# Kernel optimization log

Measured on AMD Instinct MI355X. Metric: run time of the kernel, lower is better.

The kernel has to match this reference:

```python
import jax, jax.numpy as jnp
import numpy as np

N = 100000          # nodes
E = 1600000         # edges (avg degree 16)
D_IN = 128
D_OUT = 128
K = 3               # Chebyshev order
LAMBDA_MAX = 2.0    # PyG default for sym normalization


def setup_inputs() -> dict:
    key = jax.random.key(0)
    k1, k2, k3, k4 = jax.random.split(key, 4)
    x = jax.random.normal(k1, (N, D_IN), dtype=jnp.float32)
    edge_index = jax.random.randint(k2, (2, E), 0, N, dtype=jnp.int32)
    # Glorot-ish init for the K per-order linear weights
    weight = jax.random.normal(k3, (K, D_IN, D_OUT), dtype=jnp.float32) * (1.0 / np.sqrt(D_IN))
    bias = jax.random.normal(k4, (D_OUT,), dtype=jnp.float32) * 0.01
    return {"x": x, "edge_index": edge_index, "weight": weight, "bias": bias}


def reference(x, edge_index, weight, bias):
    src, dst = edge_index[0], edge_index[1]
    n = x.shape[0]

    # remove self loops (zero their weight), symmetric normalization
    ew = jnp.where(src != dst, 1.0, 0.0).astype(x.dtype)
    deg = jax.ops.segment_sum(ew, src, num_segments=n)
    dis = jnp.where(deg > 0, jax.lax.rsqrt(jnp.maximum(deg, 1.0)), 0.0)
    norm = dis[src] * ew * dis[dst]          # D^-1/2 A D^-1/2 entries

    # scaled Laplacian T-hat = (2/lmax) L - I, L = I - A_norm
    off_w = -(2.0 / LAMBDA_MAX) * norm       # off-diagonal entries
    diag_w = 2.0 / LAMBDA_MAX - 1.0          # = 0 for lambda_max=2

    def spmm(h):  # T-hat @ h : gather-multiply-scatter over edges
        agg = jax.ops.segment_sum(off_w[:, None] * h[src], dst, num_segments=n)
        return agg + diag_w * h

    # Chebyshev recurrence: Tx_k = 2 T-hat Tx_{k-1} - Tx_{k-2}
    Tx0 = x
    out = Tx0 @ weight[0]
    Tx1 = spmm(Tx0)
    out = out + Tx1 @ weight[1]
    for k in range(2, weight.shape[0]):
        Tx2 = 2.0 * spmm(Tx1) - Tx0
        out = out + Tx2 @ weight[k]
        Tx0, Tx1 = Tx1, Tx2
    return out + bias
```

## Files before the change

### kernel.cpp

```cpp
#include <hip/hip_runtime.h>
#include <hip/hip_bf16.h>

typedef __hip_bfloat16 bf16;
typedef __attribute__((ext_vector_type(8))) short short8;
typedef __attribute__((ext_vector_type(4))) float float4v;

#define N_NODES 100000
#define M_PAD   100096
#define N_EDGES 1600000
#define D 128
#define K_CAT 384
#define BUCKET_CAP 64
#define NBIN 392
#define BIN_CAP 4608
#define CHUNK 4096

__device__ __forceinline__ float b2f(bf16 v) { return __bfloat162float(v); }
__device__ __forceinline__ bf16 f2b(float v) { return __float2bfloat16(v); }
__device__ __forceinline__ float us2f(unsigned short u) {
    unsigned int x = ((unsigned int)u) << 16;
    return __uint_as_float(x);
}

__global__ void prep_w_kernel(const float* __restrict__ w, const float* __restrict__ bias,
                              bf16* __restrict__ wT, float* __restrict__ biasf) {
    int i = blockIdx.x * blockDim.x + threadIdx.x;
    if (i < D * K_CAT) {
        int o = i / K_CAT, k = i % K_CAT;
        float v;
        if (k < 128) {
            v = w[k * D + o] - w[2 * 16384 + k * D + o];
        } else if (k < 256) {
            v = w[16384 + (k - 128) * D + o];
        } else {
            v = 2.0f * w[2 * 16384 + (k - 256) * D + o];
        }
        wT[i] = f2b(v);
    }
    if (i < D) biasf[i] = bias[i];
}

__global__ __launch_bounds__(256) void convx_kernel(const float* __restrict__ x,
                                                    bf16* __restrict__ xb) {
    int i = (blockIdx.x * 256 + threadIdx.x) * 4;
    float4 v = *(const float4*)(x + i);
    unsigned int p0 = (unsigned int)__bfloat16_as_ushort(f2b(v.x)) |
                      ((unsigned int)__bfloat16_as_ushort(f2b(v.y)) << 16);
    unsigned int p1 = (unsigned int)__bfloat16_as_ushort(f2b(v.z)) |
                      ((unsigned int)__bfloat16_as_ushort(f2b(v.w)) << 16);
    uint2 pk; pk.x = p0; pk.y = p1;
    *(uint2*)(xb + i) = pk;
}

__global__ __launch_bounds__(256) void phaseA_kernel(const int* __restrict__ src,
                                                     const int* __restrict__ dst,
                                                     int* __restrict__ gCursD,
                                                     int* __restrict__ gCursS,
                                                     unsigned int* __restrict__ gBinD,
                                                     unsigned char* __restrict__ gBinS) {
    __shared__ int histD[NBIN], histS[NBIN], cursD[NBIN], cursS[NBIN];
    int tid = threadIdx.x;
    for (int t = tid; t < NBIN; t += 256) { histD[t] = 0; histS[t] = 0; }
    __syncthreads();
    int e0 = blockIdx.x * CHUNK;
    for (int i = tid; i < CHUNK; i += 256) {
        int e = e0 + i;
        if (e >= N_EDGES) break;
        int s = src[e], d = dst[e];
        if (s == d) continue;
        atomicAdd(&histD[d >> 8], 1);
        atomicAdd(&histS[s >> 8], 1);
    }
    __syncthreads();
    for (int t = tid; t < NBIN; t += 256) {
        cursD[t] = (histD[t] > 0) ? atomicAdd(&gCursD[t], histD[t]) : 0;
        cursS[t] = (histS[t] > 0) ? atomicAdd(&gCursS[t], histS[t]) : 0;
    }
    __syncthreads();
    for (int i = tid; i < CHUNK; i += 256) {
        int e = e0 + i;
        if (e >= N_EDGES) break;
        int s = src[e], d = dst[e];
        if (s == d) continue;
        int bd = d >> 8, bs = s >> 8;
        int sd = atomicAdd(&cursD[bd], 1);
        if (sd < BIN_CAP) gBinD[(size_t)bd * BIN_CAP + sd] = ((unsigned int)s << 8) | (unsigned int)(d & 255);
        int ss = atomicAdd(&cursS[bs], 1);
        if (ss < BIN_CAP) gBinS[(size_t)bs * BIN_CAP + ss] = (unsigned char)(s & 255);
    }
}

__global__ __launch_bounds__(256) void phaseB_kernel(const int* __restrict__ gCursD,
                                                     const int* __restrict__ gCursS,
                                                     const unsigned int* __restrict__ gBinD,
                                                     const unsigned char* __restrict__ gBinS,
                                                     int* __restrict__ cnt,
                                                     float* __restrict__ dis,
                                                     int* __restrict__ bucket) {
    __shared__ int curs[256];
    int tid = threadIdx.x;
    int b = blockIdx.x;
    curs[tid] = 0;
    __syncthreads();
    if (b < NBIN) {
        int count = min(gCursD[b], BIN_CAP);
        const unsigned int* rec = gBinD + (size_t)b * BIN_CAP;
        int n0 = b << 8;
        for (int j = tid; j < count; j += 256) {
            unsigned int r = rec[j];
            int dloc = r & 255;
            int s = (int)(r >> 8);
            int slot = atomicAdd(&curs[dloc], 1);
            if (slot < BUCKET_CAP) bucket[(size_t)(n0 + dloc) * BUCKET_CAP + slot] = s;
        }
        __syncthreads();
        int n = n0 + tid;
        if (n < N_NODES) cnt[n] = curs[tid];
    } else {
        int bb = b - NBIN;
        int count = min(gCursS[bb], BIN_CAP);
        const unsigned char* rec = gBinS + (size_t)bb * BIN_CAP;
        for (int j = tid; j < count; j += 256) {
            atomicAdd(&curs[rec[j]], 1);
        }
        __syncthreads();
        int n = (bb << 8) + tid;
        if (n < N_NODES) {
            int c = curs[tid];
            dis[n] = (c > 0) ? rsqrtf((float)c) : 0.0f;
        }
    }
}

__global__ __launch_bounds__(256) void spmm_kernel(const bf16* __restrict__ h,
                                                   const float* __restrict__ dis,
                                                   const int* __restrict__ cnt,
                                                   const int* __restrict__ bucket,
                                                   bf16* __restrict__ outp) {
    int wv = threadIdx.x >> 6;
    int lane = threadIdx.x & 63;
    int n = blockIdx.x * 4 + wv;
    int c = min(cnt[n], BUCKET_CAP);
    float dn = dis[n];
    int s_l = 0;
    float w_l = 0.0f;
    if (lane < c) {
        s_l = bucket[n * BUCKET_CAP + lane];
        w_l = -dis[s_l] * dn;
    }
    int f0 = lane * 2;
    float ax = 0.0f, ay = 0.0f;
    int j = 0;
    for (; j + 4 <= c; j += 4) {
        int s0 = __shfl(s_l, j + 0), s1 = __shfl(s_l, j + 1);
        int s2 = __shfl(s_l, j + 2), s3 = __shfl(s_l, j + 3);
        float w0 = __shfl(w_l, j + 0), w1 = __shfl(w_l, j + 1);
        float w2 = __shfl(w_l, j + 2), w3 = __shfl(w_l, j + 3);
        unsigned int u0 = *(const unsigned int*)(h + (size_t)s0 * D + f0);
        unsigned int u1 = *(const unsigned int*)(h + (size_t)s1 * D + f0);
        unsigned int u2 = *(const unsigned int*)(h + (size_t)s2 * D + f0);
        unsigned int u3 = *(const unsigned int*)(h + (size_t)s3 * D + f0);
        ax += w0 * us2f((unsigned short)(u0 & 0xffff)) + w1 * us2f((unsigned short)(u1 & 0xffff))
            + w2 * us2f((unsigned short)(u2 & 0xffff)) + w3 * us2f((unsigned short)(u3 & 0xffff));
        ay += w0 * us2f((unsigned short)(u0 >> 16)) + w1 * us2f((unsigned short)(u1 >> 16))
            + w2 * us2f((unsigned short)(u2 >> 16)) + w3 * us2f((unsigned short)(u3 >> 16));
    }
    for (; j < c; j++) {
        int sj = __shfl(s_l, j);
        float wj = __shfl(w_l, j);
        unsigned int u = *(const unsigned int*)(h + (size_t)sj * D + f0);
        ax += wj * us2f((unsigned short)(u & 0xffff));
        ay += wj * us2f((unsigned short)(u >> 16));
    }
    unsigned int pk = (unsigned int)__bfloat16_as_ushort(f2b(ax)) |
                      ((unsigned int)__bfloat16_as_ushort(f2b(ay)) << 16);
    *(unsigned int*)(outp + (size_t)n * D + f0) = pk;
}

#define AS_STRIDE 40
__global__ __launch_bounds__(256) void gemm_kernel(const float* __restrict__ x,
                                                   const bf16* __restrict__ tx1,
                                                   const bf16* __restrict__ agg2,
                                                   const bf16* __restrict__ wT,
                                                   const float* __restrict__ biasf,
                                                   float* __restrict__ out) {
    __shared__ bf16 As[128 * AS_STRIDE];
    __shared__ bf16 Bs[128 * AS_STRIDE];

    int tid = threadIdx.x;
    int nb = blockIdx.x * 128;
    int w = tid >> 6;
    int lane = tid & 63;
    int lq = lane >> 4;
    int lr = lane & 15;

    float4v acc[2][8];
#pragma unroll
    for (int i = 0; i < 2; i++)
#pragma unroll
        for (int j = 0; j < 8; j++) acc[i][j] = (float4v)0.0f;

    for (int kc = 0; kc < 12; kc++) {
        int kbase = kc * 32;
        if (kc < 4) {
#pragma unroll
            for (int t = 0; t < 4; t++) {
                int c = tid + t * 256;
                int row = c >> 3;
                int off = (c & 7) * 4;
                int gr = nb + row;
                if (gr > N_NODES - 1) gr = N_NODES - 1;
                float4 v = *(const float4*)(x + (size_t)gr * D + kbase + off);
                unsigned int p0 = (unsigned int)__bfloat16_as_ushort(f2b(v.x)) |
                                  ((unsigned int)__bfloat16_as_ushort(f2b(v.y)) << 16);
                unsigned int p1 = (unsigned int)__bfloat16_as_ushort(f2b(v.z)) |
                                  ((unsigned int)__bfloat16_as_ushort(f2b(v.w)) << 16);
                uint2 pk; pk.x = p0; pk.y = p1;
                *(uint2*)(As + row * AS_STRIDE + off) = pk;
            }
        } else {
            const bf16* Asrc = (kc < 8) ? tx1 : agg2;
            int soff = (kc & 3) * 32;
#pragma unroll
            for (int t = 0; t < 2; t++) {
                int c = tid + t * 256;
                int row = c >> 2;
                int off = (c & 3) * 8;
                uint4 v = *(const uint4*)(Asrc + (size_t)(nb + row) * D + soff + off);
                *(uint4*)(As + row * AS_STRIDE + off) = v;
            }
        }
#pragma unroll
        for (int t = 0; t < 2; t++) {
            int c = tid + t * 256;
            int row = c >> 2;
            int off = (c & 3) * 8;
            uint4 v = *(const uint4*)(wT + (size_t)row * K_CAT + kbase + off);
            *(uint4*)(Bs + row * AS_STRIDE + off) = v;
        }
        __syncthreads();

        short8 af[2], bfr[8];
#pragma unroll
        for (int i = 0; i < 2; i++)
            af[i] = *(const short8*)(As + (w * 32 + i * 16 + lr) * AS_STRIDE + lq * 8);
#pragma unroll
        for (int j = 0; j < 8; j++)
            bfr[j] = *(const short8*)(Bs + (j * 16 + lr) * AS_STRIDE + lq * 8);
#pragma unroll
        for (int i = 0; i < 2; i++)
#pragma unroll
            for (int j = 0; j < 8; j++)
                acc[i][j] = __builtin_amdgcn_mfma_f32_16x16x32_bf16(af[i], bfr[j], acc[i][j], 0, 0, 0);
        __syncthreads();
    }

#pragma unroll
    for (int i = 0; i < 2; i++) {
        int rowb = nb + w * 32 + i * 16 + lq * 4;
#pragma unroll
        for (int j = 0; j < 8; j++) {
            int col = j * 16 + lr;
            float bv = biasf[col];
#pragma unroll
            for (int r = 0; r < 4; r++) {
                int row = rowb + r;
                if (row < N_NODES) out[(size_t)row * D + col] = acc[i][j][r] + bv;
            }
        }
    }
}

extern "C" void kernel_launch(void* const* d_in, const int* in_sizes, int n_in,
                              void* d_out, int out_size, void* d_ws, size_t ws_size,
                              hipStream_t stream) {
    const float* x    = (const float*)d_in[0];
    const int*   ei   = (const int*)d_in[1];
    const float* w    = (const float*)d_in[2];
    const float* bias = (const float*)d_in[3];
    float* out = (float*)d_out;

    char* p = (char*)d_ws;
    int*   cnt    = (int*)p;            p += (size_t)N_NODES * 4;
    float* dis    = (float*)p;          p += (size_t)N_NODES * 4;
    int*   gCurs  = (int*)p;            p += (size_t)2 * NBIN * 4;
    int*   bucket = (int*)p;            p += (size_t)N_NODES * BUCKET_CAP * 4;
    bf16*  buf1   = (bf16*)p;           p += (size_t)M_PAD * D * 2;
    bf16*  buf2   = (bf16*)p;           p += (size_t)M_PAD * D * 2;
    bf16*  wT     = (bf16*)p;           p += (size_t)D * K_CAT * 2;
    float* biasf  = (float*)p;          p += (size_t)D * 4;

    int*   gCursD = gCurs;
    int*   gCursS = gCurs + NBIN;
    unsigned int*  gBinD = (unsigned int*)buf1;
    unsigned char* gBinS = (unsigned char*)(gBinD + (size_t)NBIN * BIN_CAP);
    bf16* xb   = buf2;
    bf16* tx1  = buf1;
    bf16* agg2 = buf2;

    hipMemsetAsync(gCurs, 0, (size_t)2 * NBIN * 4, stream);

    prep_w_kernel<<<(D * K_CAT + 255) / 256, 256, 0, stream>>>(w, bias, wT, biasf);
    convx_kernel<<<(N_NODES * D) / 1024, 256, 0, stream>>>(x, xb);
    phaseA_kernel<<<(N_EDGES + CHUNK - 1) / CHUNK, 256, 0, stream>>>(ei, ei + N_EDGES,
                                                                     gCursD, gCursS, gBinD, gBinS);
    phaseB_kernel<<<2 * NBIN, 256, 0, stream>>>(gCursD, gCursS, gBinD, gBinS, cnt, dis, bucket);
    spmm_kernel<<<N_NODES / 4, 256, 0, stream>>>(xb, dis, cnt, bucket, tx1);
    spmm_kernel<<<N_NODES / 4, 256, 0, stream>>>(tx1, dis, cnt, bucket, agg2);
    gemm_kernel<<<M_PAD / 128, 256, 0, stream>>>(x, tx1, agg2, wT, biasf, out);
}
```

Before: 365.5 us.

## Slice features into column planes and use CSR records with precomputed edge weights

Features are stored as 8 planes of 16 columns, so each SpMM block gathers from one plane at a time, which keeps that plane's footprint small enough to stay resident in cache during the random gather. The padded 64-slot bucket is replaced by a compacted CSR-like record array built with a per-bin prefix scan, and a new kernel precomputes per-edge normalization weights. The GEMM reads its A tiles from the planar layout. The cost is an extra kernel, the edge records being read once per slice, and narrower 4-byte gathers per lane.

Measured after the change: 418.3 us. 14.4% more time.

```diff
diff --git a/kernel.cpp b/kernel.cpp
--- a/kernel.cpp
+++ b/kernel.cpp
@@ -10,16 +10,22 @@
 #define N_EDGES 1600000
 #define D 128
 #define K_CAT 384
-#define BUCKET_CAP 64
 #define NBIN 392
 #define BIN_CAP 4608
 #define CHUNK 4096
+#define NSLICE 8
+#define SLICE_F 16
+#define PLANE ((size_t)M_PAD * SLICE_F)
 
 __device__ __forceinline__ float b2f(bf16 v) { return __bfloat162float(v); }
 __device__ __forceinline__ bf16 f2b(float v) { return __float2bfloat16(v); }
 __device__ __forceinline__ float us2f(unsigned short u) {
     unsigned int x = ((unsigned int)u) << 16;
     return __uint_as_float(x);
+}
+__device__ __forceinline__ unsigned int pack2(float a, float b) {
+    return (unsigned int)__bfloat16_as_ushort(f2b(a)) |
+           ((unsigned int)__bfloat16_as_ushort(f2b(b)) << 16);
 }
 
 __global__ void prep_w_kernel(const float* __restrict__ w, const float* __restrict__ bias,
@@ -41,15 +47,26 @@
 }
 
 __global__ __launch_bounds__(256) void convx_kernel(const float* __restrict__ x,
-                                                    bf16* __restrict__ xb) {
-    int i = (blockIdx.x * 256 + threadIdx.x) * 4;
-    float4 v = *(const float4*)(x + i);
-    unsigned int p0 = (unsigned int)__bfloat16_as_ushort(f2b(v.x)) |
-                      ((unsigned int)__bfloat16_as_ushort(f2b(v.y)) << 16);
-    unsigned int p1 = (unsigned int)__bfloat16_as_ushort(f2b(v.z)) |
-                      ((unsigned int)__bfloat16_as_ushort(f2b(v.w)) << 16);
-    uint2 pk; pk.x = p0; pk.y = p1;
-    *(uint2*)(xb + i) = pk;
+                                                    bf16* __restrict__ xbT) {
+    int tid = threadIdx.x;
+    int p = tid >> 5, nloc = tid & 31;
+    int n = blockIdx.x * 32 + nloc;
+    bf16* dst = xbT + p * PLANE + (size_t)n * SLICE_F;
+    if (n < N_NODES) {
+        const float4* row = (const float4*)(x + (size_t)n * D + p * SLICE_F);
+        float4 v0 = row[0], v1 = row[1], v2 = row[2], v3 = row[3];
+        uint4 o0, o1;
+        o0.x = pack2(v0.x, v0.y); o0.y = pack2(v0.z, v0.w);
+        o0.z = pack2(v1.x, v1.y); o0.w = pack2(v1.z, v1.w);
+        o1.x = pack2(v2.x, v2.y); o1.y = pack2(v2.z, v2.w);
+        o1.z = pack2(v3.x, v3.y); o1.w = pack2(v3.z, v3.w);
+        ((uint4*)dst)[0] = o0;
+        ((uint4*)dst)[1] = o1;
+    } else {
+        uint4 z = {0, 0, 0, 0};
+        ((uint4*)dst)[0] = z;
+        ((uint4*)dst)[1] = z;
+    }
 }
 
 __global__ __launch_bounds__(256) void phaseA_kernel(const int* __restrict__ src,
@@ -95,92 +112,113 @@
                                                      const unsigned int* __restrict__ gBinD,
                                                      const unsigned char* __restrict__ gBinS,
                                                      int* __restrict__ cnt,
+                                                     int* __restrict__ recOff,
                                                      float* __restrict__ dis,
-                                                     int* __restrict__ bucket) {
-    __shared__ int curs[256];
+                                                     unsigned int* __restrict__ recS) {
+    __shared__ int hist[256], scan[256], curs[256];
     int tid = threadIdx.x;
     int b = blockIdx.x;
-    curs[tid] = 0;
+    hist[tid] = 0;
     __syncthreads();
     if (b < NBIN) {
         int count = min(gCursD[b], BIN_CAP);
         const unsigned int* rec = gBinD + (size_t)b * BIN_CAP;
-        int n0 = b << 8;
+        for (int j = tid; j < count; j += 256) atomicAdd(&hist[rec[j] & 255], 1);
+        __syncthreads();
+        int v = hist[tid];
+        scan[tid] = v;
+        __syncthreads();
+        for (int o = 1; o < 256; o <<= 1) {
+            int add = (tid >= o) ? scan[tid - o] : 0;
+            __syncthreads();
+            scan[tid] += add;
+            __syncthreads();
+        }
+        int excl = scan[tid] - v;
+        curs[tid] = excl;
+        __syncthreads();
+        unsigned int* outp = recS + (size_t)b * BIN_CAP;
         for (int j = tid; j < count; j += 256) {
             unsigned int r = rec[j];
-            int dloc = r & 255;
-            int s = (int)(r >> 8);
-            int slot = atomicAdd(&curs[dloc], 1);
-            if (slot < BUCKET_CAP) bucket[(size_t)(n0 + dloc) * BUCKET_CAP + slot] = s;
-        }
-        __syncthreads();
-        int n = n0 + tid;
-        if (n < N_NODES) cnt[n] = curs[tid];
+            int slot = atomicAdd(&curs[r & 255], 1);
+            outp[slot] = r;
+        }
+        int n = (b << 8) + tid;
+        if (n < N_NODES) { cnt[n] = v; recOff[n] = b * BIN_CAP + excl; }
     } else {
         int bb = b - NBIN;
         int count = min(gCursS[bb], BIN_CAP);
         const unsigned char* rec = gBinS + (size_t)bb * BIN_CAP;
-        for (int j = tid; j < count; j += 256) {
-            atomicAdd(&curs[rec[j]], 1);
-        }
+        for (int j = tid; j < count; j += 256) atomicAdd(&hist[rec[j]], 1);
         __syncthreads();
         int n = (bb << 8) + tid;
         if (n < N_NODES) {
-            int c = curs[tid];
+            int c = hist[tid];
             dis[n] = (c > 0) ? rsqrtf((float)c) : 0.0f;
         }
     }
 }
 
-__global__ __launch_bounds__(256) void spmm_kernel(const bf16* __restrict__ h,
+__global__ __launch_bounds__(256) void prew_kernel(const int* __restrict__ gCursD,
+                                                   const unsigned int* __restrict__ recS,
                                                    const float* __restrict__ dis,
-                                                   const int* __restrict__ cnt,
-                                                   const int* __restrict__ bucket,
-                                                   bf16* __restrict__ outp) {
-    int wv = threadIdx.x >> 6;
-    int lane = threadIdx.x & 63;
-    int n = blockIdx.x * 4 + wv;
-    int c = min(cnt[n], BUCKET_CAP);
-    float dn = dis[n];
-    int s_l = 0;
-    float w_l = 0.0f;
-    if (lane < c) {
-        s_l = bucket[n * BUCKET_CAP + lane];
-        w_l = -dis[s_l] * dn;
-    }
-    int f0 = lane * 2;
-    float ax = 0.0f, ay = 0.0f;
+                                                   float* __restrict__ recW) {
+    int b = blockIdx.x;
+    int count = min(gCursD[b], BIN_CAP);
+    const unsigned int* rp = recS + (size_t)b * BIN_CAP;
+    float* wp = recW + (size_t)b * BIN_CAP;
+    for (int j = threadIdx.x; j < count; j += 256) {
+        unsigned int r = rp[j];
+        int s = (int)(r >> 8);
+        int dn = (b << 8) + (int)(r & 255);
+        wp[j] = -dis[s] * dis[dn];
+    }
+}
+
+__global__ __launch_bounds__(256) void spmm_slice_kernel(const bf16* __restrict__ inT,
+                                                         const int* __restrict__ recOff,
+                                                         const int* __restrict__ cnt,
+                                                         const unsigned int* __restrict__ recS,
+                                                         const float* __restrict__ recW,
+                                                         bf16* __restrict__ outT) {
+    int p = blockIdx.x & 7;
+    int g = blockIdx.x >> 3;
+    int wv = threadIdx.x >> 6, lane = threadIdx.x & 63;
+    int nsub = lane >> 3, fl = lane & 7;
+    int n = g * 32 + wv * 8 + nsub;
+    const bf16* plane = inT + p * PLANE;
+    int c = 0, off = 0;
+    if (n < N_NODES) { c = cnt[n]; off = recOff[n]; }
+    float a0 = 0.0f, a1 = 0.0f;
     int j = 0;
     for (; j + 4 <= c; j += 4) {
-        int s0 = __shfl(s_l, j + 0), s1 = __shfl(s_l, j + 1);
-        int s2 = __shfl(s_l, j + 2), s3 = __shfl(s_l, j + 3);
-        float w0 = __shfl(w_l, j + 0), w1 = __shfl(w_l, j + 1);
-        float w2 = __shfl(w_l, j + 2), w3 = __shfl(w_l, j + 3);
-        unsigned int u0 = *(const unsigned int*)(h + (size_t)s0 * D + f0);
-        unsigned int u1 = *(const unsigned int*)(h + (size_t)s1 * D + f0);
-        unsigned int u2 = *(const unsigned int*)(h + (size_t)s2 * D + f0);
-        unsigned int u3 = *(const unsigned int*)(h + (size_t)s3 * D + f0);
-        ax += w0 * us2f((unsigned short)(u0 & 0xffff)) + w1 * us2f((unsigned short)(u1 & 0xffff))
+        unsigned int r0 = recS[off + j + 0], r1 = recS[off + j + 1];
+        unsigned int r2 = recS[off + j + 2], r3 = recS[off + j + 3];
+        float w0 = recW[off + j + 0], w1 = recW[off + j + 1];
+        float w2 = recW[off + j + 2], w3 = recW[off + j + 3];
+        unsigned int u0 = *(const unsigned int*)(plane + (size_t)(r0 >> 8) * SLICE_F + fl * 2);
+        unsigned int u1 = *(const unsigned int*)(plane + (size_t)(r1 >> 8) * SLICE_F + fl * 2);
+        unsigned int u2 = *(const unsigned int*)(plane + (size_t)(r2 >> 8) * SLICE_F + fl * 2);
+        unsigned int u3 = *(const unsigned int*)(plane + (size_t)(r3 >> 8) * SLICE_F + fl * 2);
+        a0 += w0 * us2f((unsigned short)(u0 & 0xffff)) + w1 * us2f((unsigned short)(u1 & 0xffff))
             + w2 * us2f((unsigned short)(u2 & 0xffff)) + w3 * us2f((unsigned short)(u3 & 0xffff));
-        ay += w0 * us2f((unsigned short)(u0 >> 16)) + w1 * us2f((unsigned short)(u1 >> 16))
+        a1 += w0 * us2f((unsigned short)(u0 >> 16)) + w1 * us2f((unsigned short)(u1 >> 16))
             + w2 * us2f((unsigned short)(u2 >> 16)) + w3 * us2f((unsigned short)(u3 >> 16));
     }
     for (; j < c; j++) {
-        int sj = __shfl(s_l, j);
-        float wj = __shfl(w_l, j);
-        unsigned int u = *(const unsigned int*)(h + (size_t)sj * D + f0);
-        ax += wj * us2f((unsigned short)(u & 0xffff));
-        ay += wj * us2f((unsigned short)(u >> 16));
-    }
-    unsigned int pk = (unsigned int)__bfloat16_as_ushort(f2b(ax)) |
-                      ((unsigned int)__bfloat16_as_ushort(f2b(ay)) << 16);
-    *(unsigned int*)(outp + (size_t)n * D + f0) = pk;
+        unsigned int r = recS[off + j];
+        float w = recW[off + j];
+        unsigned int u = *(const unsigned int*)(plane + (size_t)(r >> 8) * SLICE_F + fl * 2);
+        a0 += w * us2f((unsigned short)(u & 0xffff));
+        a1 += w * us2f((unsigned short)(u >> 16));
+    }
+    *(unsigned int*)(outT + p * PLANE + (size_t)n * SLICE_F + fl * 2) = pack2(a0, a1);
 }
 
 #define AS_STRIDE 40
 __global__ __launch_bounds__(256) void gemm_kernel(const float* __restrict__ x,
-                                                   const bf16* __restrict__ tx1,
-                                                   const bf16* __restrict__ agg2,
+                                                   const bf16* __restrict__ tx1T,
+                                                   const bf16* __restrict__ agg2T,
                                                    const bf16* __restrict__ wT,
                                                    const float* __restrict__ biasf,
                                                    float* __restrict__ out) {
@@ -211,23 +249,21 @@
                 int gr = nb + row;
                 if (gr > N_NODES - 1) gr = N_NODES - 1;
                 float4 v = *(const float4*)(x + (size_t)gr * D + kbase + off);
-                unsigned int p0 = (unsigned int)__bfloat16_as_ushort(f2b(v.x)) |
-                                  ((unsigned int)__bfloat16_as_ushort(f2b(v.y)) << 16);
-                unsigned int p1 = (unsigned int)__bfloat16_as_ushort(f2b(v.z)) |
-                                  ((unsigned int)__bfloat16_as_ushort(f2b(v.w)) << 16);
-                uint2 pk; pk.x = p0; pk.y = p1;
+                uint2 pk;
+                pk.x = pack2(v.x, v.y);
+                pk.y = pack2(v.z, v.w);
                 *(uint2*)(As + row * AS_STRIDE + off) = pk;
             }
         } else {
-            const bf16* Asrc = (kc < 8) ? tx1 : agg2;
-            int soff = (kc & 3) * 32;
-#pragma unroll
-            for (int t = 0; t < 2; t++) {
-                int c = tid + t * 256;
-                int row = c >> 2;
-                int off = (c & 3) * 8;
-                uint4 v = *(const uint4*)(Asrc + (size_t)(nb + row) * D + soff + off);
-                *(uint4*)(As + row * AS_STRIDE + off) = v;
+            const bf16* base = (kc < 8) ? tx1T : agg2T;
+            int m2 = (kc & 3) * 2;
+#pragma unroll
+            for (int sr = 0; sr < 2; sr++) {
+                const bf16* chunkp = base + (size_t)(m2 + sr) * PLANE + (size_t)nb * SLICE_F;
+                uint4 v = *(const uint4*)(chunkp + tid * 8);
+                int row = tid >> 1;
+                int col = sr * 16 + (tid & 1) * 8;
+                *(uint4*)(As + row * AS_STRIDE + col) = v;
             }
         }
 #pragma unroll
@@ -283,29 +319,33 @@
     char* p = (char*)d_ws;
     int*   cnt    = (int*)p;            p += (size_t)N_NODES * 4;
     float* dis    = (float*)p;          p += (size_t)N_NODES * 4;
+    int*   recOff = (int*)p;            p += (size_t)N_NODES * 4;
     int*   gCurs  = (int*)p;            p += (size_t)2 * NBIN * 4;
-    int*   bucket = (int*)p;            p += (size_t)N_NODES * BUCKET_CAP * 4;
-    bf16*  buf1   = (bf16*)p;           p += (size_t)M_PAD * D * 2;
-    bf16*  buf2   = (bf16*)p;           p += (size_t)M_PAD * D * 2;
+    unsigned int* recS = (unsigned int*)p;  p += (size_t)NBIN * BIN_CAP * 4;
+    float* recW   = (float*)p;          p += (size_t)NBIN * BIN_CAP * 4;
+    bf16*  R1     = (bf16*)p;           p += PLANE * NSLICE * 2;
+    bf16*  R2     = (bf16*)p;           p += PLANE * NSLICE * 2;
     bf16*  wT     = (bf16*)p;           p += (size_t)D * K_CAT * 2;
     float* biasf  = (float*)p;          p += (size_t)D * 4;
 
-    int*   gCursD = gCurs;
-    int*   gCursS = gCurs + NBIN;
-    unsigned int*  gBinD = (unsigned int*)buf1;
+    int* gCursD = gCurs;
+    int* gCursS = gCurs + NBIN;
+    unsigned int*  gBinD = (unsigned int*)R2;
     unsigned char* gBinS = (unsigned char*)(gBinD + (size_t)NBIN * BIN_CAP);
-    bf16* xb   = buf2;
-    bf16* tx1  = buf1;
-    bf16* agg2 = buf2;
+    bf16* xbT   = R1;
+    bf16* tx1T  = R2;
+    bf16* agg2T = R1;
 
     hipMemsetAsync(gCurs, 0, (size_t)2 * NBIN * 4, stream);
 
     prep_w_kernel<<<(D * K_CAT + 255) / 256, 256, 0, stream>>>(w, bias, wT, biasf);
-    convx_kernel<<<(N_NODES * D) / 1024, 256, 0, stream>>>(x, xb);
+    convx_kernel<<<M_PAD / 32, 256, 0, stream>>>(x, xbT);
     phaseA_kernel<<<(N_EDGES + CHUNK - 1) / CHUNK, 256, 0, stream>>>(ei, ei + N_EDGES,
                                                                      gCursD, gCursS, gBinD, gBinS);
-    phaseB_kernel<<<2 * NBIN, 256, 0, stream>>>(gCursD, gCursS, gBinD, gBinS, cnt, dis, bucket);
-    spmm_kernel<<<N_NODES / 4, 256, 0, stream>>>(xb, dis, cnt, bucket, tx1);
-    spmm_kernel<<<N_NODES / 4, 256, 0, stream>>>(tx1, dis, cnt, bucket, agg2);
-    gemm_kernel<<<M_PAD / 128, 256, 0, stream>>>(x, tx1, agg2, wT, biasf, out);
-}
+    phaseB_kernel<<<2 * NBIN, 256, 0, stream>>>(gCursD, gCursS, gBinD, gBinS,
+                                                cnt, recOff, dis, recS);
+    prew_kernel<<<NBIN, 256, 0, stream>>>(gCursD, recS, dis, recW);
+    spmm_slice_kernel<<<(M_PAD / 32) * 8, 256, 0, stream>>>(xbT, recOff, cnt, recS, recW, tx1T);
+    spmm_slice_kernel<<<(M_PAD / 32) * 8, 256, 0, stream>>>(tx1T, recOff, cnt, recS, recW, agg2T);
+    gemm_kernel<<<M_PAD / 128, 256, 0, stream>>>(x, tx1T, agg2T, wT, biasf, out);
+}
```
